# Performance work log

Hardware: AMD Instinct MI355X
Metric: run time of the kernel (lower is better)

Reference implementation:

```python
import jax, jax.numpy as jnp
import numpy as np

B, L, D = 8, 2048, 512


def setup_inputs() -> dict:
    key = jax.random.key(0)
    ks = jax.random.split(key, 9)
    s = 1.0 / np.sqrt(D)
    x = jax.random.normal(ks[0], (B, L, D), dtype=jnp.float32)
    Wq = jax.random.uniform(ks[1], (D, D), jnp.float32, -s, s)
    bq = jax.random.uniform(ks[2], (D,), jnp.float32, -s, s)
    Wk = jax.random.uniform(ks[3], (D, D), jnp.float32, -s, s)
    bk = jax.random.uniform(ks[4], (D,), jnp.float32, -s, s)
    Wv = jax.random.uniform(ks[5], (D, D), jnp.float32, -s, s)
    bv = jax.random.uniform(ks[6], (D,), jnp.float32, -s, s)
    Wo = jax.random.uniform(ks[7], (D, D), jnp.float32, -s, s)
    bo = jax.random.uniform(ks[8], (D,), jnp.float32, -s, s)
    return {"x": x, "Wq": Wq, "bq": bq, "Wk": Wk, "bk": bk,
            "Wv": Wv, "bv": bv, "Wo": Wo, "bo": bo}


def reference(x, Wq, bq, Wk, bk, Wv, bv, Wo, bo):
    # Projections then rfft along sequence axis -> complex [B, F, D], F = L//2+1
    Q = jnp.fft.rfft(x @ Wq + bq, axis=1)
    K = jnp.fft.rfft(x @ Wk + bk, axis=1)
    V = jnp.fft.rfft(x @ Wv + bv, axis=1)
    scale = K.shape[-1] ** (-0.5)
    # Complex attention scores over frequency bins: [B, F, F]
    att = jnp.einsum('bfd,bgd->bfg', Q, K) * scale
    attn = jax.nn.softmax(jnp.abs(att), axis=-1)
    context = jnp.einsum('bfg,bgd->bfd', attn.astype(Q.dtype), V)
    context = jnp.fft.irfft(context, n=x.shape[1], axis=1)  # [B, L, D] real
    return context @ Wo + bo
```

## Files before the change

kernel.cpp:

```cpp
#include <hip/hip_runtime.h>
#include <hip/hip_bf16.h>
#include <math.h>

typedef __hip_bfloat16 bf16;
typedef __attribute__((ext_vector_type(8))) short short8;
typedef __attribute__((ext_vector_type(4))) float f32x4;

#define BB 8
#define LL 2048
#define DD 512
#define FF 1025
#define GP 1088
#define FPAD 1152
#define PSTRIDE 589824
#define ATT_SCALE 0.04419417382415922f

__device__ __forceinline__ float b2f(bf16 v) { return __bfloat162float(v); }
__device__ __forceinline__ bf16  f2b(float v) { return __float2bfloat16(v); }
__device__ __forceinline__ float s2f(short s) { bf16 t; *reinterpret_cast<short*>(&t) = s; return b2f(t); }
__device__ __forceinline__ unsigned pk2f(float a, float b) {
    bf16 ha = f2b(a), hb = f2b(b);
    return (unsigned)*(unsigned short*)&ha | ((unsigned)*(unsigned short*)&hb << 16);
}

#define MFMA16(a, b, c) __builtin_amdgcn_mfma_f32_16x16x32_bf16((a), (b), (c), 0, 0, 0)

__device__ __forceinline__ short8 neg8(short8 v) {
    short8 r;
    #pragma unroll
    for (int t = 0; t < 8; ++t) r[t] = (short)(v[t] ^ (short)0x8000);
    return r;
}

typedef __attribute__((address_space(1))) const unsigned int gu32;
typedef __attribute__((address_space(3))) unsigned int lu32;
__device__ __forceinline__ void gl16(const void* g, void* l) {
    __builtin_amdgcn_global_load_lds((gu32*)g, (lu32*)l, 16, 0, 0);
}

template<bool F32>
__device__ __forceinline__ float ldin(const void* p, size_t i) {
    if (F32) return ((const float*)p)[i];
    else     return b2f(((const bf16*)p)[i]);
}

__global__ __launch_bounds__(256) void detect_dtype(const unsigned short* __restrict__ x,
                                                    int* __restrict__ flag)
{
    __shared__ int cnt[256];
    int c = 0;
    for (int i = threadIdx.x; i < 4096; i += 256) {
        const int e = (x[i] >> 7) & 0xFF;
        c += (e >= 100 && e <= 150) ? 1 : 0;
    }
    cnt[threadIdx.x] = c;
    __syncthreads();
    for (int s = 128; s; s >>= 1) {
        if (threadIdx.x < s) cnt[threadIdx.x] += cnt[threadIdx.x + s];
        __syncthreads();
    }
    if (threadIdx.x == 0) *flag = (cnt[0] < 3400) ? 1 : 0;
}

__global__ __launch_bounds__(256) void prep_bias(const void* __restrict__ b0,
                                                 const void* __restrict__ b1,
                                                 const void* __restrict__ b2,
                                                 const void* __restrict__ b3,
                                                 float* __restrict__ bias_f,
                                                 const int* __restrict__ flag)
{
    const int idx = blockIdx.x * 256 + threadIdx.x;
    const int which = idx >> 9, i = idx & 511;
    const void* src = which == 0 ? b0 : (which == 1 ? b1 : (which == 2 ? b2 : b3));
    bias_f[idx] = (*flag) ? ldin<true>(src, i) : ldin<false>(src, i);
}

__global__ __launch_bounds__(256) void split_w_t(const void* __restrict__ W0,
                                                 const void* __restrict__ W1,
                                                 const void* __restrict__ W2,
                                                 const void* __restrict__ W3,
                                                 bf16* __restrict__ WT,
                                                 const int* __restrict__ flag)
{
    const int z = blockIdx.z;
    const void* W = z == 0 ? W0 : (z == 1 ? W1 : (z == 2 ? W2 : W3));
    bf16* Wh = WT + (size_t)z * 524288;
    const int k0 = blockIdx.x * 32, n0 = blockIdx.y * 32;
    const bool f32 = (*flag) != 0;
    __shared__ float Tl[32][33];
    for (int it = 0; it < 4; ++it) {
        const int idx = it * 256 + threadIdx.x;
        const int lk = idx >> 5, ln = idx & 31;
        Tl[lk][ln] = f32 ? ldin<true>(W, (size_t)(k0 + lk) * 512 + n0 + ln)
                         : ldin<false>(W, (size_t)(k0 + lk) * 512 + n0 + ln);
    }
    __syncthreads();
    for (int it = 0; it < 4; ++it) {
        const int idx = it * 256 + threadIdx.x;
        const int ln = idx >> 5, lk = idx & 31;
        Wh[(size_t)(n0 + ln) * 512 + k0 + lk] = f2b(Tl[lk][ln]);
    }
}

__device__ __forceinline__ int shx(int i, int c) {
    const int x = (i << 2) | c;
    return x ^ (((x >> 6) & 3) << 2);
}

__device__ __forceinline__ void fft_decode(int flat, int& b, int& dp) {
    const int c8 = flat & 7;
    const int s  = (flat >> 3) & 1;
    const int pp = flat >> 4;
    const int idx = c8 * 32 + pp;
    b  = idx >> 5;
    dp = ((idx & 31) << 1) | s;
}

__device__ __forceinline__ void fill_twl(float2* twl, int tid) {
    for (int idx = tid; idx < 2047; idx += 512) {
        const int l2 = 31 - __builtin_clz((unsigned)(2047 - idx));
        const int m = 1 << l2;
        const int k = idx - 2048 + 2 * m;
        float s, c2;
        __sincosf(-3.14159265358979f * (float)k / (float)m, &s, &c2);
        twl[idx] = make_float2(c2, s);
    }
}

__global__ __launch_bounds__(512) void rfft_x(const void* __restrict__ x,
                                              bf16* __restrict__ Xh,
                                              const int* __restrict__ flag)
{
    int b, dp;
    fft_decode(blockIdx.x, b, dp);
    const int d0 = dp * 8;
    __shared__ float2 sh[8192];
    __shared__ float2 twl[2048];
    const int tid = threadIdx.x;
    const int c = tid & 3;

    if (*flag) {
        const float* base = (const float*)x + (size_t)b * 2048 * 512 + d0;
        #pragma unroll
        for (int it = 0; it < 8; ++it) {
            const int idx = it * 512 + tid;
            const int l = idx >> 1, fq = idx & 1;
            const float4 v = *(const float4*)(base + (size_t)l * 512 + fq * 4);
            sh[shx(l, fq * 2)]     = make_float2(v.x, v.y);
            sh[shx(l, fq * 2 + 1)] = make_float2(v.z, v.w);
        }
    } else {
        const bf16* base = (const bf16*)x + (size_t)b * 2048 * 512 + d0;
        #pragma unroll
        for (int it = 0; it < 4; ++it) {
            const int l = it * 512 + tid;
            const short8 v = *(const short8*)(base + (size_t)l * 512);
            #pragma unroll
            for (int q = 0; q < 4; ++q)
                sh[shx(l, q)] = make_float2(s2f(v[2 * q]), s2f(v[2 * q + 1]));
        }
    }
    fill_twl(twl, tid);
    __syncthreads();

    const int jb = tid >> 2;
    #pragma unroll
    for (int lsm = 10; lsm >= 0; --lsm) {
        const int m = 1 << lsm;
        const int base = 2048 - (m << 1);
        #pragma unroll
        for (int r = 0; r < 8; ++r) {
            const int j  = jb + 128 * r;
            const int k  = j & (m - 1);
            const int i1 = ((j & ~(m - 1)) << 1) | k;
            const int i2 = i1 + m;
            const float2 w = twl[base + k];
            const float cw = w.x, sw = w.y;
            const float2 a  = sh[shx(i1, c)];
            const float2 bb = sh[shx(i2, c)];
            sh[shx(i1, c)] = make_float2(a.x + bb.x, a.y + bb.y);
            const float dx = a.x - bb.x, dy = a.y - bb.y;
            sh[shx(i2, c)] = make_float2(dx * cw - dy * sw, dx * sw + dy * cw);
        }
        __syncthreads();
    }

    const int fb = tid >> 2;
    const size_t pan_re = (size_t)(b * 64 + dp) * FPAD;
    const size_t pan_im = pan_re + (size_t)512 * FPAD;
    auto dorow = [&](int f) {
        const int rf = __brev((unsigned)f) >> 21;
        const int rc = __brev((unsigned)((2048 - f) & 2047)) >> 21;
        const float2 Zf = sh[shx(rf, c)];
        const float2 Zc = sh[shx(rc, c)];
        const float x1r = 0.5f * (Zf.x + Zc.x);
        const float x1i = 0.5f * (Zf.y - Zc.y);
        const float x2r = 0.5f * (Zf.y + Zc.y);
        const float x2i = -0.5f * (Zf.x - Zc.x);
        const size_t ro_re = (pan_re + f) * 8 + 2 * c;
        const size_t ro_im = (pan_im + f) * 8 + 2 * c;
        *(unsigned*)&Xh[ro_re] = pk2f(x1r, x2r);
        *(unsigned*)&Xh[ro_im] = pk2f(x1i, x2i);
    };
    #pragma unroll
    for (int it = 0; it < 8; ++it)
        dorow(fb * 8 + it);
    if (tid < 4) dorow(1024);

    if (tid < 254) {
        const int f = FF + (tid >> 1);
        const int w = tid & 1;
        const size_t off = (((size_t)(w * 512 + b * 64 + dp)) * FPAD + f) * 8;
        short8 z = {};
        *(short8*)&Xh[off] = z;
    }
}

__global__ __launch_bounds__(256) void proj_all(const bf16* __restrict__ Xh,
                                                const bf16* __restrict__ WT,
                                                const float* __restrict__ bias_f,
                                                bf16* __restrict__ Q,
                                                bf16* __restrict__ K,
                                                bf16* __restrict__ Vct)
{
    const int flat = blockIdx.x;
    const bool isV = flat < 576;
    int t, ny, z;
    if (isV) { t = flat >> 2; ny = flat & 3; z = 2; }
    else { const int idx = flat - 576; t = idx >> 3; z = (idx >> 2) & 1; ny = idx & 3; }

    const int pb = t / 9;
    const int f0 = (t - pb * 9) * 128;
    const int plane = pb >> 3, b = pb & 7;
    const int n0 = ny * 128;
    const int tid = threadIdx.x, wv = tid >> 6, lane = tid & 63;
    const int wm = (wv >> 1) * 64, wn = (wv & 1) * 64;
    const size_t pbase = (size_t)pb * PSTRIDE;

    const bf16* Bh = WT + (size_t)z * 524288;
    const float* bias = bias_f + z * 512;

    __shared__ __align__(1024) bf16 SH[16384];
    typedef bf16 (*t64)[64];
    t64 Al = (t64)SH;
    t64 Bl = (t64)(SH + 8192);

    const int r8 = lane >> 3;
    const int sl = lane & 7;
    const int q  = sl ^ r8;
    const int r16 = lane & 15, cc = lane >> 4;
    const int rs8 = r16 & 7;
    const int nn2 = lane & 15, rq = (lane >> 4) * 4;

    f32x4 acc[4][4] = {};
    for (int kt = 0; kt < 512; kt += 64) {
        #pragma unroll
        for (int c2 = 0; c2 < 4; ++c2) {
            const int chunk = wv * 4 + c2;
            const int row = chunk * 8 + r8;
            gl16(&Xh[pbase + ((size_t)((kt >> 3) + q) * FPAD + f0 + row) * 8],
                 (char*)SH + chunk * 1024);
            gl16(&Bh[(size_t)(n0 + row) * 512 + kt + q * 8],
                 (char*)SH + 16384 + chunk * 1024);
        }
        __syncthreads();

        #pragma unroll
        for (int kk = 0; kk < 2; ++kk) {
            short8 af[4], bfr[4];
            const int sa = ((kk * 4 + cc) ^ rs8) * 8;
            #pragma unroll
            for (int i = 0; i < 4; ++i) {
                af[i]  = *(const short8*)&Al[wm + i * 16 + r16][sa];
                bfr[i] = *(const short8*)&Bl[wn + i * 16 + r16][sa];
            }
            #pragma unroll
            for (int i = 0; i < 4; ++i)
                #pragma unroll
                for (int j = 0; j < 4; ++j)
                    acc[i][j] = MFMA16(af[i], bfr[j], acc[i][j]);
        }
        __syncthreads();
    }

    if (!isV) {
        bf16* dst = z == 0 ? Q : K;
        const size_t SPQ = (size_t)BB * FF * DD;
        #pragma unroll
        for (int i = 0; i < 4; ++i)
            #pragma unroll
            for (int j = 0; j < 4; ++j) {
                const int col = n0 + wn + j * 16 + nn2;
                #pragma unroll
                for (int r = 0; r < 4; ++r) {
                    const int f = f0 + wm + i * 16 + rq + r;
                    if (f < FF) {
                        float v = acc[i][j][r];
                        if (plane == 0 && f == 0) v += 2048.0f * bias[col];
                        const int swz = ((f >> 1) & 3) << 3;
                        dst[(size_t)plane * SPQ + ((size_t)(b * FF + f)) * 512 + (col ^ swz)] = f2b(v);
                    }
                }
            }
    } else {
        bf16* T = SH;
        #pragma unroll
        for (int i = 0; i < 4; ++i)
            #pragma unroll
            for (int j = 0; j < 4; ++j) {
                const int col_l = wn + j * 16 + nn2;
                #pragma unroll
                for (int r = 0; r < 4; ++r) {
                    const int row_l = wm + i * 16 + rq + r;
                    const int f = f0 + row_l;
                    float v = (f < FF) ? acc[i][j][r] : 0.f;
                    if (plane == 0 && f == 0) v += 2048.0f * bias[n0 + col_l];
                    T[col_l * 128 + (row_l ^ ((col_l & 15) << 3))] = f2b(v);
                }
            }
        __syncthreads();

        const int nl = tid >> 1, half = tid & 1;
        const size_t gbase = ((size_t)(b * 1024 + plane * 512 + n0 + nl)) * GP + f0;
        #pragma unroll
        for (int a = 0; a < 8; ++a) {
            const int fl = half * 64 + a * 8;
            if (f0 + fl < GP) {
                const short8 v8 = *(const short8*)&T[nl * 128 + (fl ^ ((nl & 15) << 3))];
                *(short8*)&Vct[gbase + fl] = v8;
            }
        }
    }
}

__global__ __launch_bounds__(256, 2) void att_mfma(const bf16* __restrict__ Asp,
                                                   const bf16* __restrict__ Bsp,
                                                   float* __restrict__ att)
{
    const size_t SP = (size_t)BB * FF * DD;
    const int flat = blockIdx.x;
    const int b    = flat & 7;
    const int slot = flat >> 3;
    const int grp  = slot / 51;
    const int rem  = slot % 51;
    const int g    = rem / 3;
    const int r3   = rem % 3;
    const int ft   = grp * 3 + r3;
    const int f0 = ft * 128, g0 = g * 64;

    const int tid = threadIdx.x;
    const int wv = tid >> 6, lane = tid & 63;
    const int wvf = wv >> 1, wvg = wv & 1;

    __shared__ __align__(1024) char LB[24576];
    bf16 (*Al)[128][32] = (bf16(*)[128][32])LB;
    bf16 (*Bl)[64][32]  = (bf16(*)[64][32])(LB + 16384);

    f32x4 accr[4][2] = {}; f32x4 acci[4][2] = {};

    const int r16 = lane & 15, cc = lane >> 4;
    const int rpos = (cc ^ ((r16 >> 1) & 3)) * 8;
    const size_t abase = (size_t)(b * FF + f0) * 512;
    const size_t bbase = (size_t)(b * FF + g0) * 512;
    const int lrow = lane >> 2;
    const int lcol = (lane & 3) * 8;

    for (int kt = 0; kt < 512; kt += 32) {
        #pragma unroll
        for (int c2 = 0; c2 < 4; ++c2) {
            const int chunk = wv * 4 + c2;
            const int pl = chunk >> 3, rg = chunk & 7;
            const int row = rg * 16 + lrow;
            gl16(&Asp[(size_t)pl * SP + abase + (size_t)row * 512 + kt + lcol],
                 LB + chunk * 1024);
        }
        #pragma unroll
        for (int c2 = 0; c2 < 2; ++c2) {
            const int chunk = wv * 2 + c2;
            const int pl = chunk >> 2, rg = chunk & 3;
            const int row = rg * 16 + lrow;
            gl16(&Bsp[(size_t)pl * SP + bbase + (size_t)row * 512 + kt + lcol],
                 LB + 16384 + chunk * 1024);
        }
        __syncthreads();

        short8 aA[4][2], bB[2][2], nb[2];
        #pragma unroll
        for (int i = 0; i < 4; ++i) {
            const int row = wvf * 64 + i * 16 + r16;
            #pragma unroll
            for (int pl = 0; pl < 2; ++pl)
                aA[i][pl] = *(const short8*)&Al[pl][row][rpos];
        }
        #pragma unroll
        for (int j = 0; j < 2; ++j) {
            const int row = wvg * 32 + j * 16 + r16;
            #pragma unroll
            for (int pl = 0; pl < 2; ++pl)
                bB[j][pl] = *(const short8*)&Bl[pl][row][rpos];
            nb[j] = neg8(bB[j][1]);
        }
        #pragma unroll
        for (int i = 0; i < 4; ++i)
            #pragma unroll
            for (int j = 0; j < 2; ++j) {
                accr[i][j] = MFMA16(aA[i][0], bB[j][0], accr[i][j]);
                accr[i][j] = MFMA16(aA[i][1], nb[j],    accr[i][j]);
                acci[i][j] = MFMA16(aA[i][0], bB[j][1], acci[i][j]);
                acci[i][j] = MFMA16(aA[i][1], bB[j][0], acci[i][j]);
            }
        __syncthreads();
    }

    const int rq = (lane >> 4) * 4;
    #pragma unroll
    for (int i = 0; i < 4; ++i)
        #pragma unroll
        for (int j = 0; j < 2; ++j)
            #pragma unroll
            for (int r = 0; r < 4; ++r) {
                const int f = f0 + wvf * 64 + i * 16 + rq + r;
                const int gg = g0 + wvg * 32 + j * 16 + r16;
                if (f < FF && gg < FF) {
                    const float ar = accr[i][j][r];
                    const float ai = acci[i][j][r];
                    att[((size_t)(b * FF + f)) * FF + gg] = ATT_SCALE * sqrtf(ar * ar + ai * ai);
                }
            }
}

__global__ __launch_bounds__(256) void softmax_rows(const float* __restrict__ att,
                                                    bf16* __restrict__ att16)
{
    const int row = blockIdx.x;
    const float* p = att + (size_t)row * FF;
    bf16* q = att16 + (size_t)row * GP;
    const int tid = threadIdx.x;
    const int lane = tid & 63, wid = tid >> 6;
    __shared__ float srow[1028];
    __shared__ float red[4];

    float m = -1e30f;
    for (int i = tid; i < FF; i += 256) {
        const float v = p[i];
        srow[i] = v;
        m = fmaxf(m, v);
    }
    #pragma unroll
    for (int o = 32; o; o >>= 1) m = fmaxf(m, __shfl_down(m, o));
    if (lane == 0) red[wid] = m;
    __syncthreads();
    m = fmaxf(fmaxf(red[0], red[1]), fmaxf(red[2], red[3]));
    __syncthreads();

    float s = 0.f;
    for (int i = tid; i < FF; i += 256) s += expf(srow[i] - m);
    #pragma unroll
    for (int o = 32; o; o >>= 1) s += __shfl_down(s, o);
    if (lane == 0) red[wid] = s;
    __syncthreads();
    s = red[0] + red[1] + red[2] + red[3];
    const float inv = 1.f / s;
    for (int i = tid; i < GP; i += 256)
        q[i] = f2b(i < FF ? expf(srow[i] - m) * inv : 0.f);
}

__global__ __launch_bounds__(256, 2) void ctx_mfma(const bf16* __restrict__ att16,
                                                   const bf16* __restrict__ Vct,
                                                   bf16* __restrict__ Csp)
{
    const int flat = blockIdx.x;
    const int b    = flat & 7;
    const int slot = flat >> 3;
    const int ft   = slot >> 4;
    const int nt   = slot & 15;
    const int f0 = ft * 128, n0 = nt * 64;

    const int tid = threadIdx.x;
    const int wv = tid >> 6, lane = tid & 63;
    const int wvf = wv >> 1, wvg = wv & 1;

    __shared__ __align__(16) bf16 Al[128][64];
    __shared__ __align__(16) bf16 Bl[64][64];

    f32x4 acc[4][2] = {};
    const int srow8 = tid >> 3, sq8 = tid & 7;
    const int r16 = lane & 15, cc = lane >> 4;
    const int rs8 = r16 & 7;

    for (int kt = 0; kt < GP; kt += 64) {
        #pragma unroll
        for (int p = 0; p < 4; ++p) {
            const int row = p * 32 + srow8;
            const int pos = (sq8 ^ (row & 7)) * 8;
            uint4 av = make_uint4(0, 0, 0, 0);
            if (f0 + row < FF)
                av = *(const uint4*)&att16[((size_t)(b * FF + f0 + row)) * GP + kt + sq8 * 8];
            *(uint4*)&Al[row][pos] = av;
        }
        #pragma unroll
        for (int p = 0; p < 2; ++p) {
            const int row = p * 32 + srow8;
            const int pos = (sq8 ^ (row & 7)) * 8;
            *(uint4*)&Bl[row][pos] =
                *(const uint4*)&Vct[((size_t)(b * 1024 + n0 + row)) * GP + kt + sq8 * 8];
        }
        __syncthreads();

        #pragma unroll
        for (int kk = 0; kk < 2; ++kk) {
            short8 aA[4], bB[2];
            const int sa = ((kk * 4 + cc) ^ rs8) * 8;
            #pragma unroll
            for (int i = 0; i < 4; ++i)
                aA[i] = *(const short8*)&Al[wvf * 64 + i * 16 + r16][sa];
            #pragma unroll
            for (int j = 0; j < 2; ++j)
                bB[j] = *(const short8*)&Bl[wvg * 32 + j * 16 + r16][sa];
            #pragma unroll
            for (int i = 0; i < 4; ++i)
                #pragma unroll
                for (int j = 0; j < 2; ++j)
                    acc[i][j] = MFMA16(aA[i], bB[j], acc[i][j]);
        }
        __syncthreads();
    }

    const int rq = (lane >> 4) * 4;
    #pragma unroll
    for (int i = 0; i < 4; ++i)
        #pragma unroll
        for (int j = 0; j < 2; ++j)
            #pragma unroll
            for (int r = 0; r < 4; ++r) {
                const int f = f0 + wvf * 64 + i * 16 + rq + r;
                const int n = n0 + wvg * 32 + j * 16 + r16;
                if (f < FF) {
                    const int d = n & 511, pl = n >> 9;
                    Csp[((size_t)(pl * 8 + b) * FPAD + f) * 512 + d] = f2b(acc[i][j][r]);
                }
            }
}

__global__ __launch_bounds__(256) void out_mfma_freq(const bf16* __restrict__ A,
                                                     const bf16* __restrict__ BhT,
                                                     float* __restrict__ CwR,
                                                     float* __restrict__ CwI)
{
    const int t = blockIdx.x;
    const int pb = t / 9;
    const int f0 = (t - pb * 9) * 128;
    const int plane = pb >> 3, b = pb & 7;
    const int m0 = t * 128, n0 = blockIdx.y * 64;
    const int tid = threadIdx.x, wv = tid >> 6, lane = tid & 63;
    const int wvf = wv >> 1, wvg = wv & 1;

    __shared__ __align__(16) bf16 Al[128][32];
    __shared__ __align__(16) bf16 Bl[64][32];

    f32x4 acc[4][2] = {};
    const int srow = tid >> 2, sq = tid & 3;
    const int r16 = lane & 15, cc = lane >> 4;
    const int rpos = (cc ^ ((r16 >> 1) & 3)) * 8;

    for (int kt = 0; kt < 512; kt += 32) {
        #pragma unroll
        for (int p = 0; p < 2; ++p) {
            const int r = p * 64 + srow;
            const int pos = (sq ^ ((r >> 1) & 3)) * 8;
            *(uint4*)&Al[r][pos] = *(const uint4*)&A[(size_t)(m0 + r) * 512 + kt + sq * 8];
        }
        {
            const int pos = (sq ^ ((srow >> 1) & 3)) * 8;
            *(uint4*)&Bl[srow][pos] = *(const uint4*)&BhT[(size_t)(n0 + srow) * 512 + kt + sq * 8];
        }
        __syncthreads();

        short8 af[4], bfr[2];
        #pragma unroll
        for (int i = 0; i < 4; ++i)
            af[i] = *(const short8*)&Al[wvf * 64 + i * 16 + r16][rpos];
        #pragma unroll
        for (int j = 0; j < 2; ++j)
            bfr[j] = *(const short8*)&Bl[wvg * 32 + j * 16 + r16][rpos];
        #pragma unroll
        for (int i = 0; i < 4; ++i)
            #pragma unroll
            for (int j = 0; j < 2; ++j)
                acc[i][j] = MFMA16(af[i], bfr[j], acc[i][j]);
        __syncthreads();
    }

    float* dst = plane ? CwI : CwR;
    const int nn2 = lane & 15, rq = (lane >> 4) * 4;
    #pragma unroll
    for (int i = 0; i < 4; ++i)
        #pragma unroll
        for (int j = 0; j < 2; ++j) {
            const int col = n0 + wvg * 32 + j * 16 + nn2;
            #pragma unroll
            for (int r = 0; r < 4; ++r) {
                const int f = f0 + wvf * 64 + i * 16 + rq + r;
                if (f < FF)
                    dst[((size_t)(b * FF + f)) * 512 + col] = acc[i][j][r];
            }
        }
}

__global__ __launch_bounds__(512) void irfft8(const float* __restrict__ CwR,
                                              const float* __restrict__ CwI,
                                              void* __restrict__ out,
                                              const float* __restrict__ bias_f,
                                              const int* __restrict__ flag)
{
    int b, dp;
    fft_decode(blockIdx.x, b, dp);
    const int d0 = dp * 8;
    __shared__ float2 sh[8192];
    __shared__ float2 twl[2048];
    const int tid = threadIdx.x;
    const int c = tid & 3, fb = tid >> 2;

    for (int it = 0; it < 9; ++it) {
        const int f = fb + 128 * it;
        if (f < FF) {
            const size_t off = ((size_t)(b * FF + f)) * 512 + d0 + 2 * c;
            const float2 vr = *(const float2*)(CwR + off);
            const float2 vi = *(const float2*)(CwI + off);
            float c1x = vr.x, c1y = vi.x, c2x = vr.y, c2y = vi.y;
            if (f == 0 || f == 1024) { c1y = 0.f; c2y = 0.f; }
            sh[shx(f, c)] = make_float2(c1x - c2y, c1y + c2x);
            if (f >= 1 && f <= 1023)
                sh[shx(2048 - f, c)] = make_float2(c1x + c2y, c2x - c1y);
        }
    }
    fill_twl(twl, tid);
    __syncthreads();

    const int jb = fb;
    #pragma unroll
    for (int lsm = 10; lsm >= 0; --lsm) {
        const int m = 1 << lsm;
        const int base = 2048 - (m << 1);
        #pragma unroll
        for (int r = 0; r < 8; ++r) {
            const int j  = jb + 128 * r;
            const int k  = j & (m - 1);
            const int i1 = ((j & ~(m - 1)) << 1) | k;
            const int i2 = i1 + m;
            const float2 w = twl[base + k];
            const float cw = w.x, sw = -w.y;
            const float2 a  = sh[shx(i1, c)];
            const float2 bb = sh[shx(i2, c)];
            sh[shx(i1, c)] = make_float2(a.x + bb.x, a.y + bb.y);
            const float dx = a.x - bb.x, dy = a.y - bb.y;
            sh[shx(i2, c)] = make_float2(dx * cw - dy * sw, dx * sw + dy * cw);
        }
        __syncthreads();
    }

    const float sc = 1.0f / 2048.0f;
    const float bo0 = bias_f[1536 + d0 + 2 * c];
    const float bo1 = bias_f[1536 + d0 + 2 * c + 1];
    const bool f32o = (*flag) != 0;
    const int lb = tid >> 2;
    #pragma unroll
    for (int it = 0; it < 16; ++it) {
        const int l  = lb * 16 + it;
        const int rl = __brev((unsigned)l) >> 21;
        const float2 z = sh[shx(rl, c)];
        const float o0 = z.x * sc + bo0;
        const float o1 = z.y * sc + bo1;
        const size_t off = ((size_t)(b * 2048 + l)) * 512 + d0 + 2 * c;
        if (f32o) {
            *(float2*)((float*)out + off) = make_float2(o0, o1);
        } else {
            __hip_bfloat162 h;
            h.x = f2b(o0); h.y = f2b(o1);
            *(__hip_bfloat162*)((bf16*)out + off) = h;
        }
    }
}

extern "C" void kernel_launch(void* const* d_in, const int* in_sizes, int n_in,
                              void* d_out, int out_size, void* d_ws, size_t ws_size,
                              hipStream_t stream)
{
    const void* x  = d_in[0];
    const void* Wq = d_in[1]; const void* bq = d_in[2];
    const void* Wk = d_in[3]; const void* bk = d_in[4];
    const void* Wv = d_in[5]; const void* bv = d_in[6];
    const void* Wo = d_in[7]; const void* bo = d_in[8];

    char* ws = (char*)d_ws;
    char* pA = ws;
    char* pB = pA + 33652736;
    char* pC = pB + 37748736;
    char* pD = pC + 17039360;
    char* pE = pD + 17039360;
    char* pW = pE + 17825792;

    float*  attn = (float*)pA;
    bf16*   Xh   = (bf16*)pB;
    bf16*   att16= (bf16*)pB;
    bf16*   Csp  = (bf16*)(pB + 17843200);
    bf16*   Asp  = (bf16*)pC;
    bf16*   Bsp  = (bf16*)pD;
    float*  CwR  = (float*)pC;
    float*  CwI  = (float*)pD;
    bf16*   Vct  = (bf16*)pE;
    bf16*   WT   = (bf16*)pW;
    float*  bias_f = (float*)(pW + 4194304);
    int*    flag = (int*)(pW + 4194304 + 8192);

    detect_dtype<<<1, 256, 0, stream>>>((const unsigned short*)x, flag);
    prep_bias<<<8, 256, 0, stream>>>(bq, bk, bv, bo, bias_f, flag);
    split_w_t<<<dim3(16, 16, 4), 256, 0, stream>>>(Wq, Wk, Wv, Wo, WT, flag);
    rfft_x<<<dim3(512), 512, 0, stream>>>(x, Xh, flag);
    proj_all<<<dim3(1728), 256, 0, stream>>>(Xh, WT, bias_f, Asp, Bsp, Vct);
    att_mfma<<<dim3(1224), 256, 0, stream>>>(Asp, Bsp, attn);
    softmax_rows<<<dim3(BB * FF), 256, 0, stream>>>(attn, att16);
    ctx_mfma<<<dim3(1152), 256, 0, stream>>>(att16, Vct, Csp);
    out_mfma_freq<<<dim3(144, 8), 256, 0, stream>>>(Csp, WT + 3 * 524288, CwR, CwI);
    irfft8<<<dim3(512), 512, 0, stream>>>(CwR, CwI, d_out, bias_f, flag);
}
```

Before: 341.7 us.

## Use direct-to-LDS loads, deeper K tiles across GEMMs, cache softmax exps

Four kernels are reworked at once. The complex attention-score GEMM and the output GEMM now stage 64-wide K tiles per barrier instead of 32, halving the barrier count. The context and output GEMMs switch from register-staged global-to-LDS copies to direct global-to-LDS (gl16) loads with an XOR swizzle. The context kernel drops its f<FF row guard, so padding rows beyond FF are read unmasked, which can run past the end of the buffer for the last batch. Separately, proj_all gets a min-4-blocks occupancy hint, and softmax stores exp values in shared memory instead of recomputing them.

```diff
diff --git a/kernel.cpp b/kernel.cpp
--- a/kernel.cpp
+++ b/kernel.cpp
@@ -216,12 +216,12 @@
     }
 }
 
-__global__ __launch_bounds__(256) void proj_all(const bf16* __restrict__ Xh,
-                                                const bf16* __restrict__ WT,
-                                                const float* __restrict__ bias_f,
-                                                bf16* __restrict__ Q,
-                                                bf16* __restrict__ K,
-                                                bf16* __restrict__ Vct)
+__global__ __launch_bounds__(256, 4) void proj_all(const bf16* __restrict__ Xh,
+                                                   const bf16* __restrict__ WT,
+                                                   const float* __restrict__ bias_f,
+                                                   bf16* __restrict__ Q,
+                                                   bf16* __restrict__ K,
+                                                   bf16* __restrict__ Vct)
 {
     const int flat = blockIdx.x;
     const bool isV = flat < 576;
@@ -352,9 +352,7 @@
     const int wv = tid >> 6, lane = tid & 63;
     const int wvf = wv >> 1, wvg = wv & 1;
 
-    __shared__ __align__(1024) char LB[24576];
-    bf16 (*Al)[128][32] = (bf16(*)[128][32])LB;
-    bf16 (*Bl)[64][32]  = (bf16(*)[64][32])(LB + 16384);
+    __shared__ __align__(1024) char LB[49152];
 
     f32x4 accr[4][2] = {}; f32x4 acci[4][2] = {};
 
@@ -365,50 +363,57 @@
     const int lrow = lane >> 2;
     const int lcol = (lane & 3) * 8;
 
-    for (int kt = 0; kt < 512; kt += 32) {
+    for (int kt = 0; kt < 512; kt += 64) {
+        #pragma unroll
+        for (int c2 = 0; c2 < 8; ++c2) {
+            const int chunk = wv * 8 + c2;
+            const int half = chunk >> 4;
+            const int pl = (chunk >> 3) & 1, rg = chunk & 7;
+            const int row = rg * 16 + lrow;
+            gl16(&Asp[(size_t)pl * SP + abase + (size_t)row * 512 + kt + half * 32 + lcol],
+                 LB + half * 16384 + ((pl << 3) | rg) * 1024);
+        }
         #pragma unroll
         for (int c2 = 0; c2 < 4; ++c2) {
             const int chunk = wv * 4 + c2;
-            const int pl = chunk >> 3, rg = chunk & 7;
+            const int half = chunk >> 3;
+            const int pl = (chunk >> 2) & 1, rg = chunk & 3;
             const int row = rg * 16 + lrow;
-            gl16(&Asp[(size_t)pl * SP + abase + (size_t)row * 512 + kt + lcol],
-                 LB + chunk * 1024);
-        }
-        #pragma unroll
-        for (int c2 = 0; c2 < 2; ++c2) {
-            const int chunk = wv * 2 + c2;
-            const int pl = chunk >> 2, rg = chunk & 3;
-            const int row = rg * 16 + lrow;
-            gl16(&Bsp[(size_t)pl * SP + bbase + (size_t)row * 512 + kt + lcol],
-                 LB + 16384 + chunk * 1024);
-        }
-        __syncthreads();
-
-        short8 aA[4][2], bB[2][2], nb[2];
-        #pragma unroll
-        for (int i = 0; i < 4; ++i) {
-            const int row = wvf * 64 + i * 16 + r16;
-            #pragma unroll
-            for (int pl = 0; pl < 2; ++pl)
-                aA[i][pl] = *(const short8*)&Al[pl][row][rpos];
-        }
-        #pragma unroll
-        for (int j = 0; j < 2; ++j) {
-            const int row = wvg * 32 + j * 16 + r16;
-            #pragma unroll
-            for (int pl = 0; pl < 2; ++pl)
-                bB[j][pl] = *(const short8*)&Bl[pl][row][rpos];
-            nb[j] = neg8(bB[j][1]);
-        }
-        #pragma unroll
-        for (int i = 0; i < 4; ++i)
+            gl16(&Bsp[(size_t)pl * SP + bbase + (size_t)row * 512 + kt + half * 32 + lcol],
+                 LB + 32768 + half * 8192 + ((pl << 2) | rg) * 1024);
+        }
+        __syncthreads();
+
+        #pragma unroll
+        for (int kk = 0; kk < 2; ++kk) {
+            bf16 (*Al)[128][32] = (bf16(*)[128][32])(LB + kk * 16384);
+            bf16 (*Bl)[64][32]  = (bf16(*)[64][32])(LB + 32768 + kk * 8192);
+            short8 aA[4][2], bB[2][2], nb[2];
+            #pragma unroll
+            for (int i = 0; i < 4; ++i) {
+                const int row = wvf * 64 + i * 16 + r16;
+                #pragma unroll
+                for (int pl = 0; pl < 2; ++pl)
+                    aA[i][pl] = *(const short8*)&Al[pl][row][rpos];
+            }
             #pragma unroll
             for (int j = 0; j < 2; ++j) {
-                accr[i][j] = MFMA16(aA[i][0], bB[j][0], accr[i][j]);
-                accr[i][j] = MFMA16(aA[i][1], nb[j],    accr[i][j]);
-                acci[i][j] = MFMA16(aA[i][0], bB[j][1], acci[i][j]);
-                acci[i][j] = MFMA16(aA[i][1], bB[j][0], acci[i][j]);
-            }
+                const int row = wvg * 32 + j * 16 + r16;
+                #pragma unroll
+                for (int pl = 0; pl < 2; ++pl)
+                    bB[j][pl] = *(const short8*)&Bl[pl][row][rpos];
+                nb[j] = neg8(bB[j][1]);
+            }
+            #pragma unroll
+            for (int i = 0; i < 4; ++i)
+                #pragma unroll
+                for (int j = 0; j < 2; ++j) {
+                    accr[i][j] = MFMA16(aA[i][0], bB[j][0], accr[i][j]);
+                    accr[i][j] = MFMA16(aA[i][1], nb[j],    accr[i][j]);
+                    acci[i][j] = MFMA16(aA[i][0], bB[j][1], acci[i][j]);
+                    acci[i][j] = MFMA16(aA[i][1], bB[j][0], acci[i][j]);
+                }
+        }
         __syncthreads();
     }
 
@@ -454,7 +459,11 @@
     __syncthreads();
 
     float s = 0.f;
-    for (int i = tid; i < FF; i += 256) s += expf(srow[i] - m);
+    for (int i = tid; i < FF; i += 256) {
+        const float e = expf(srow[i] - m);
+        srow[i] = e;
+        s += e;
+    }
     #pragma unroll
     for (int o = 32; o; o >>= 1) s += __shfl_down(s, o);
     if (lane == 0) red[wid] = s;
@@ -462,7 +471,7 @@
     s = red[0] + red[1] + red[2] + red[3];
     const float inv = 1.f / s;
     for (int i = tid; i < GP; i += 256)
-        q[i] = f2b(i < FF ? expf(srow[i] - m) * inv : 0.f);
+        q[i] = f2b(i < FF ? srow[i] * inv : 0.f);
 }
 
 __global__ __launch_bounds__(256, 2) void ctx_mfma(const bf16* __restrict__ att16,
@@ -480,30 +489,30 @@
     const int wv = tid >> 6, lane = tid & 63;
     const int wvf = wv >> 1, wvg = wv & 1;
 
-    __shared__ __align__(16) bf16 Al[128][64];
-    __shared__ __align__(16) bf16 Bl[64][64];
+    __shared__ __align__(1024) bf16 SH[12288];
+    typedef bf16 (*t64)[64];
+    t64 Al = (t64)SH;
+    t64 Bl = (t64)(SH + 8192);
 
     f32x4 acc[4][2] = {};
-    const int srow8 = tid >> 3, sq8 = tid & 7;
+    const int r8 = lane >> 3, sl = lane & 7, q = sl ^ r8;
     const int r16 = lane & 15, cc = lane >> 4;
     const int rs8 = r16 & 7;
 
     for (int kt = 0; kt < GP; kt += 64) {
         #pragma unroll
-        for (int p = 0; p < 4; ++p) {
-            const int row = p * 32 + srow8;
-            const int pos = (sq8 ^ (row & 7)) * 8;
-            uint4 av = make_uint4(0, 0, 0, 0);
-            if (f0 + row < FF)
-                av = *(const uint4*)&att16[((size_t)(b * FF + f0 + row)) * GP + kt + sq8 * 8];
-            *(uint4*)&Al[row][pos] = av;
-        }
-        #pragma unroll
-        for (int p = 0; p < 2; ++p) {
-            const int row = p * 32 + srow8;
-            const int pos = (sq8 ^ (row & 7)) * 8;
-            *(uint4*)&Bl[row][pos] =
-                *(const uint4*)&Vct[((size_t)(b * 1024 + n0 + row)) * GP + kt + sq8 * 8];
+        for (int c2 = 0; c2 < 4; ++c2) {
+            const int chunk = wv * 4 + c2;
+            const int row = chunk * 8 + r8;
+            gl16(&att16[((size_t)(b * FF + f0 + row)) * GP + kt + q * 8],
+                 (char*)SH + chunk * 1024);
+        }
+        #pragma unroll
+        for (int c2 = 0; c2 < 2; ++c2) {
+            const int chunk = wv * 2 + c2;
+            const int row = chunk * 8 + r8;
+            gl16(&Vct[((size_t)(b * 1024 + n0 + row)) * GP + kt + q * 8],
+                 (char*)SH + 16384 + chunk * 1024);
         }
         __syncthreads();
 
@@ -555,39 +564,49 @@
     const int tid = threadIdx.x, wv = tid >> 6, lane = tid & 63;
     const int wvf = wv >> 1, wvg = wv & 1;
 
-    __shared__ __align__(16) bf16 Al[128][32];
-    __shared__ __align__(16) bf16 Bl[64][32];
+    __shared__ __align__(1024) bf16 SH[12288];
+    typedef bf16 (*t64)[64];
+    t64 Al = (t64)SH;
+    t64 Bl = (t64)(SH + 8192);
 
     f32x4 acc[4][2] = {};
-    const int srow = tid >> 2, sq = tid & 3;
+    const int r8 = lane >> 3, sl = lane & 7, q = sl ^ r8;
     const int r16 = lane & 15, cc = lane >> 4;
-    const int rpos = (cc ^ ((r16 >> 1) & 3)) * 8;
-
-    for (int kt = 0; kt < 512; kt += 32) {
-        #pragma unroll
-        for (int p = 0; p < 2; ++p) {
-            const int r = p * 64 + srow;
-            const int pos = (sq ^ ((r >> 1) & 3)) * 8;
-            *(uint4*)&Al[r][pos] = *(const uint4*)&A[(size_t)(m0 + r) * 512 + kt + sq * 8];
-        }
-        {
-            const int pos = (sq ^ ((srow >> 1) & 3)) * 8;
-            *(uint4*)&Bl[srow][pos] = *(const uint4*)&BhT[(size_t)(n0 + srow) * 512 + kt + sq * 8];
-        }
-        __syncthreads();
-
-        short8 af[4], bfr[2];
-        #pragma unroll
-        for (int i = 0; i < 4; ++i)
-            af[i] = *(const short8*)&Al[wvf * 64 + i * 16 + r16][rpos];
-        #pragma unroll
-        for (int j = 0; j < 2; ++j)
-            bfr[j] = *(const short8*)&Bl[wvg * 32 + j * 16 + r16][rpos];
-        #pragma unroll
-        for (int i = 0; i < 4; ++i)
+    const int rs8 = r16 & 7;
+
+    for (int kt = 0; kt < 512; kt += 64) {
+        #pragma unroll
+        for (int c2 = 0; c2 < 4; ++c2) {
+            const int chunk = wv * 4 + c2;
+            const int row = chunk * 8 + r8;
+            gl16(&A[(size_t)(m0 + row) * 512 + kt + q * 8],
+                 (char*)SH + chunk * 1024);
+        }
+        #pragma unroll
+        for (int c2 = 0; c2 < 2; ++c2) {
+            const int chunk = wv * 2 + c2;
+            const int row = chunk * 8 + r8;
+            gl16(&BhT[(size_t)(n0 + row) * 512 + kt + q * 8],
+                 (char*)SH + 16384 + chunk * 1024);
+        }
+        __syncthreads();
+
+        #pragma unroll
+        for (int kk = 0; kk < 2; ++kk) {
+            short8 af[4], bfr[2];
+            const int sa = ((kk * 4 + cc) ^ rs8) * 8;
+            #pragma unroll
+            for (int i = 0; i < 4; ++i)
+                af[i] = *(const short8*)&Al[wvf * 64 + i * 16 + r16][sa];
             #pragma unroll
             for (int j = 0; j < 2; ++j)
-                acc[i][j] = MFMA16(af[i], bfr[j], acc[i][j]);
+                bfr[j] = *(const short8*)&Bl[wvg * 32 + j * 16 + r16][sa];
+            #pragma unroll
+            for (int i = 0; i < 4; ++i)
+                #pragma unroll
+                for (int j = 0; j < 2; ++j)
+                    acc[i][j] = MFMA16(af[i], bfr[j], acc[i][j]);
+        }
         __syncthreads();
     }
 
```

Result: faster. 320.8 us (-6.1%).
